# Optimization experiments

Measured on AMD Instinct MI355X. Metric: run time of the kernel, lower is better.

## Reference

```python
import jax, jax.numpy as jnp
import numpy as np

N_NODES = 50000
N_EDGES = 300000
D = 256          # in_dim = out_dim (residual)
DE = 256         # edge relation dim
K = 2            # num_kgs
H = 4            # heads
L = 2            # layers
DH = D // H


def _routed_linear(x, W, b, idx):
    # x:[E,din], W:[K,din,dout], b:[K,dout], idx:[E] in [0,K)
    # Compute all K branches (K is tiny) then select per edge.
    outs = jnp.einsum('ed,kdo->keo', x, W) + b[:, None, :]
    return outs[idx, jnp.arange(idx.shape[0])]


def _layernorm(x, g, b):
    mu = jnp.mean(x, axis=-1, keepdims=True)
    var = jnp.mean(jnp.square(x - mu), axis=-1, keepdims=True)
    return (x - mu) * jax.lax.rsqrt(var + 1e-5) * g + b


def _mga_layer(h, src, dst, kg_src, kg_dst, beta, rel,
               ln_g, ln_b, Wt, bt, Wq, bq, Wk, bk):
    N = h.shape[0]
    E = src.shape[0]
    residual = h
    hn = _layernorm(h, ln_g, ln_b)
    x_j = hn[src]                       # [E,D] gathered source feats
    x_i = hn[dst]                       # [E,D] gathered target feats
    # per-edge KG-routed transfer of concatenated (x_j, relation emb)
    xj_t = jax.nn.gelu(_routed_linear(jnp.concatenate([x_j, rel], axis=1), Wt, bt, kg_src),
                       approximate=False)
    q = _routed_linear(x_i, Wq, bq, kg_dst).reshape(E, H, DH)
    k = _routed_linear(xj_t, Wk, bk, kg_src).reshape(E, H, DH)
    # per-edge multi-head dot product, scaled by edge_beta_r then 1/sqrt(dh)
    att = jnp.sum(q * k, axis=-1) * beta[:, None] / jnp.sqrt(jnp.asarray(DH, h.dtype))  # [E,H]
    # scatter-softmax over incoming edges of each target node
    m = jax.ops.segment_max(att, dst, num_segments=N)          # [N,H]
    e = jnp.exp(att - m[dst])
    denom = jax.ops.segment_sum(e, dst, num_segments=N)        # [N,H]
    a = e / (denom[dst] + 1e-16)                                # [E,H]
    msg = (a[:, :, None] * xj_t.reshape(E, H, DH)).reshape(E, D)
    aggr = jax.ops.segment_sum(msg, dst, num_segments=N)        # [N,D]
    return residual + jax.nn.gelu(aggr, approximate=False)


def setup_inputs() -> dict:
    key = jax.random.key(0)
    ks = jax.random.split(key, 10)
    x = jax.random.normal(ks[0], (N_NODES, D), dtype=jnp.float32)
    edge_index = jax.random.randint(ks[1], (2, N_EDGES), 0, N_NODES, dtype=jnp.int32)
    edge_kg_index = jax.random.randint(ks[2], (2, N_EDGES), 0, K, dtype=jnp.int32)
    edge_beta_r = jax.random.uniform(ks[3], (N_EDGES,), dtype=jnp.float32)
    edge_rel_emb = jax.random.normal(ks[4], (N_EDGES, DE), dtype=jnp.float32)
    return {
        'x': x,
        'edge_index': edge_index,
        'edge_kg_index': edge_kg_index,
        'edge_beta_r': edge_beta_r,
        'edge_rel_emb': edge_rel_emb,
        'ln_g': jnp.ones((L, D), jnp.float32),
        'ln_b': jnp.zeros((L, D), jnp.float32),
        'Wt': jax.random.normal(ks[5], (L, K, D + DE, D), jnp.float32) / np.sqrt(D + DE),
        'bt': jnp.zeros((L, K, D), jnp.float32),
        'Wq': jax.random.normal(ks[6], (L, K, D, D), jnp.float32) / np.sqrt(D),
        'bq': jnp.zeros((L, K, D), jnp.float32),
        'Wk': jax.random.normal(ks[7], (L, K, D, D), jnp.float32) / np.sqrt(D),
        'bk': jnp.zeros((L, K, D), jnp.float32),
    }


def reference(x, edge_index, edge_kg_index, edge_beta_r, edge_rel_emb,
              ln_g, ln_b, Wt, bt, Wq, bq, Wk, bk):
    src, dst = edge_index[0], edge_index[1]          # j (source), i (target)
    kg_src, kg_dst = edge_kg_index[0], edge_kg_index[1]
    h = x  # dropout is identity in eval mode
    for l in range(L):
        h = _mga_layer(h, src, dst, kg_src, kg_dst, edge_beta_r, edge_rel_emb,
                       ln_g[l], ln_b[l], Wt[l], bt[l], Wq[l], bq[l], Wk[l], bk[l])
    return h
```

## Files before the change

### kernel.cpp

```cpp
#include <hip/hip_runtime.h>
#include <hip/hip_bf16.h>

#define NN 50000
#define NE 300000
#define DD 256
#define NCHUNK 293

typedef __hip_bfloat16 bf16;
typedef __attribute__((ext_vector_type(8))) short bf16x8;
typedef __attribute__((ext_vector_type(4))) float f32x4;

__device__ __forceinline__ float bf2f(bf16 v) { return __bfloat162float(v); }
__device__ __forceinline__ unsigned short f2b(float v) {
    bf16 t = __float2bfloat16(v);
    return *reinterpret_cast<unsigned short*>(&t);
}
__device__ __forceinline__ float b2f_bits(unsigned short u) {
    return __uint_as_float(((unsigned)u) << 16);
}
__device__ __forceinline__ float gelu_f(float v) {
    float v2 = v * v;
    float z  = v * fmaf(v2, 0.044715f, 1.0f) * 0.7978845608f;
    float e  = __expf(2.0f * z);
    float th = 1.0f - 2.0f / (e + 1.0f);
    return 0.5f * v * (1.0f + th);
}
__device__ __forceinline__ void gl2lds16(const uint4* g, uint4* l) {
    __builtin_amdgcn_global_load_lds(
        (const __attribute__((address_space(1))) void*)g,
        (__attribute__((address_space(3))) void*)l, 16, 0, 0);
}

__global__ void part_count(const int* __restrict__ kg, int* __restrict__ bcnt) {
    int base = blockIdx.x * 1024;
    __shared__ int wc[4];
    int t = threadIdx.x, wave = t >> 6, lane = t & 63;
    int cnt = 0;
    #pragma unroll
    for (int s = 0; s < 4; ++s) {
        int j = base + s * 256 + t;
        int is0 = (j < NE && kg[j] == 0) ? 1 : 0;
        unsigned long long m = __ballot(is0);
        if (lane == 0) cnt += __popcll(m);
    }
    if (lane == 0) wc[wave] = cnt;
    __syncthreads();
    if (t == 0) bcnt[blockIdx.x] = wc[0] + wc[1] + wc[2] + wc[3];
}

__global__ __launch_bounds__(512) void part_scan(const int* __restrict__ bcnt,
                                                 int* __restrict__ bofs,
                                                 int* __restrict__ meta, int n) {
    __shared__ int tmp[512];
    int t = threadIdx.x;
    int v = (t < n) ? bcnt[t] : 0;
    tmp[t] = v;
    __syncthreads();
    #pragma unroll
    for (int off = 1; off < 512; off <<= 1) {
        int u = (t >= off) ? tmp[t - off] : 0;
        __syncthreads();
        tmp[t] += u;
        __syncthreads();
    }
    if (t < n) bofs[t] = tmp[t] - v;
    if (t == n - 1) meta[0] = tmp[t];
}

__global__ void part_scatter(const int* __restrict__ kg, const int* __restrict__ bofs,
                             const int* __restrict__ meta, int* __restrict__ perm) {
    int base = blockIdx.x * 1024;
    int c0 = meta[0];
    __shared__ int wz[4];
    int t = threadIdx.x, wave = t >> 6, lane = t & 63;
    int zrun = bofs[blockIdx.x];
    for (int s = 0; s < 4; ++s) {
        int j = base + s * 256 + t;
        int valid = j < NE;
        int is0 = (valid && kg[j] == 0) ? 1 : 0;
        unsigned long long m = __ballot(is0);
        int zb = __popcll(m & ((1ull << lane) - 1ull));
        if (lane == 0) wz[wave] = __popcll(m);
        __syncthreads();
        int wbefore = 0;
        for (int w = 0; w < wave; ++w) wbefore += wz[w];
        int zeros_before = zrun + wbefore + zb;
        if (valid) {
            int pos = is0 ? zeros_before : (c0 + (j - zeros_before));
            perm[pos] = j;
        }
        int stepz = wz[0] + wz[1] + wz[2] + wz[3];
        __syncthreads();
        zrun += stepz;
    }
}

__global__ void deg_hist(const int* __restrict__ dst, int* __restrict__ deg) {
    int i = blockIdx.x * blockDim.x + threadIdx.x;
    if (i < NE) atomicAdd(&deg[dst[i]], 1);
}

__global__ __launch_bounds__(1024) void scan_big(const int* __restrict__ in,
                                                 int* __restrict__ ofs,
                                                 int* __restrict__ cur, int n) {
    __shared__ int part[1024];
    int t = threadIdx.x;
    int C = (n + 1023) >> 10;
    int base = t * C;
    int s = 0;
    for (int j = 0; j < C; ++j) { int idx = base + j; if (idx < n) s += in[idx]; }
    part[t] = s;
    __syncthreads();
    #pragma unroll
    for (int off = 1; off < 1024; off <<= 1) {
        int u = (t >= off) ? part[t - off] : 0;
        __syncthreads();
        part[t] += u;
        __syncthreads();
    }
    int run = (t == 0) ? 0 : part[t - 1];
    for (int j = 0; j < C; ++j) {
        int idx = base + j;
        if (idx < n) {
            ofs[idx] = run;
            if (cur) cur[idx] = run;
            run += in[idx];
        }
    }
    if (t == 1023) ofs[n] = part[1023];
}

__global__ void csr_fill(const int* __restrict__ dst, int* __restrict__ cur,
                         int* __restrict__ eid) {
    int i = blockIdx.x * blockDim.x + threadIdx.x;
    if (i < NE) {
        int p = atomicAdd(&cur[dst[i]], 1);
        eid[p] = i;
    }
}

__global__ void f2b_vec_kernel(const float* __restrict__ in, ushort* __restrict__ out, long n4) {
    long i0 = (long)blockIdx.x * blockDim.x + threadIdx.x;
    long stride = (long)gridDim.x * blockDim.x;
    for (long i = i0; i < n4; i += stride) {
        float4 v = ((const float4*)in)[i];
        ushort4 o;
        o.x = f2b(v.x); o.y = f2b(v.y); o.z = f2b(v.z); o.w = f2b(v.w);
        ((ushort4*)out)[i] = o;
    }
}

__global__ void transpose_w_kernel(const float* __restrict__ in, ushort* __restrict__ out,
                                   int shift, long total) {
    long i0 = (long)blockIdx.x * blockDim.x + threadIdx.x;
    long stride = (long)gridDim.x * blockDim.x;
    long dmask = ((long)1 << shift) - 1;
    for (long i = i0; i < total; i += stride) {
        long d = i & dmask;
        long rest = i >> shift;
        long o = rest & 255;
        long s = rest >> 8;
        out[i] = f2b(in[((s << shift) + d) * 256 + o]);
    }
}

__global__ void fill_kernel(float* __restrict__ p, float v, int n) {
    for (int i = blockIdx.x * blockDim.x + threadIdx.x; i < n; i += gridDim.x * blockDim.x)
        p[i] = v;
}

__global__ __launch_bounds__(256) void lnx_kernel(const float* __restrict__ x,
        const float* __restrict__ g, const float* __restrict__ b,
        float* __restrict__ h, bf16* __restrict__ hn) {
    int n = blockIdx.x * 4 + (threadIdx.x >> 6);
    if (n >= NN) return;
    int t = threadIdx.x & 63;
    float4 v = ((const float4*)(x + (size_t)n * DD))[t];
    ((float4*)(h + (size_t)n * DD))[t] = v;
    float s  = v.x + v.y + v.z + v.w;
    float s2 = v.x * v.x + v.y * v.y + v.z * v.z + v.w * v.w;
    #pragma unroll
    for (int off = 32; off; off >>= 1) {
        s  += __shfl_down(s, off);
        s2 += __shfl_down(s2, off);
    }
    s = __shfl(s, 0); s2 = __shfl(s2, 0);
    float mu  = s * (1.f / DD);
    float var = s2 * (1.f / DD) - mu * mu;
    float rs  = rsqrtf(var + 1e-5f);
    float vv[4] = {v.x, v.y, v.z, v.w};
    ushort4 pk;
    unsigned short* pku = (unsigned short*)&pk;
    #pragma unroll
    for (int j = 0; j < 4; ++j) {
        int c = t * 4 + j;
        pku[j] = f2b((vv[j] - mu) * rs * g[c] + b[c]);
    }
    ((ushort4*)(hn + (size_t)n * DD))[t] = pk;
}

__global__ __launch_bounds__(512) void nodeq_mfma(
        const bf16* __restrict__ hn,
        const ushort* __restrict__ WqT, const float* __restrict__ bq,
        const ushort* __restrict__ WtT, const float* __restrict__ bt,
        ushort* __restrict__ qn, ushort* __restrict__ hw) {
    __shared__ uint4 xh[64 * 32];
    __shared__ float bqs[2][256], bts[2][256];
    int t = threadIdx.x;
    int n0 = blockIdx.x * 64;
    int wave = t >> 6, lane = t & 63;
    if (t < 256) { bqs[0][t] = bq[t]; bqs[1][t] = bq[256 + t]; }
    else { int c = t & 255; bts[0][c] = bt[c]; bts[1][c] = bt[256 + c]; }
    const uint4* hn4 = (const uint4*)hn;
    #pragma unroll
    for (int j = 0; j < 4; ++j) {
        int pr = wave * 4 + j;
        int r2 = pr * 2 + (lane >> 5);
        int node = n0 + r2; if (node >= NN) node = NN - 1;
        int s = lane & 31;
        gl2lds16(hn4 + (size_t)node * 32 + (s ^ (r2 & 7)), &xh[pr * 64]);
    }
    __syncthreads();
    int lr = lane & 15, lg = lane >> 4;
    const char* xhb = (const char*)xh;
    f32x4 acc[2][2][4];
    #pragma unroll
    for (int b = 0; b < 2; ++b)
        #pragma unroll
        for (int m = 0; m < 2; ++m)
            #pragma unroll
            for (int n = 0; n < 4; ++n) acc[b][m][n] = (f32x4){0.f, 0.f, 0.f, 0.f};
    {
        const ushort* tr0 = WtT + (size_t)(wave * 32 + lr) * 512 + lg * 8;
        const ushort* tr1 = WtT + (size_t)(wave * 32 + 16 + lr) * 512 + lg * 8;
        #pragma unroll
        for (int kk = 0; kk < 8; ++kk) {
            bf16x8 a00 = *(const bf16x8*)(tr0 + kk * 32);
            bf16x8 a01 = *(const bf16x8*)(tr1 + kk * 32);
            bf16x8 a10 = *(const bf16x8*)(tr0 + 131072 + kk * 32);
            bf16x8 a11 = *(const bf16x8*)(tr1 + 131072 + kk * 32);
            bf16x8 bfr[4];
            #pragma unroll
            for (int n = 0; n < 4; ++n) {
                int r = n * 16 + lr;
                bfr[n] = *(const bf16x8*)(xhb + r * 512 + (((kk * 4 + lg) ^ (r & 7)) << 4));
            }
            #pragma unroll
            for (int n = 0; n < 4; ++n) {
                acc[0][0][n] = __builtin_amdgcn_mfma_f32_16x16x32_bf16(a00, bfr[n], acc[0][0][n], 0, 0, 0);
                acc[0][1][n] = __builtin_amdgcn_mfma_f32_16x16x32_bf16(a01, bfr[n], acc[0][1][n], 0, 0, 0);
                acc[1][0][n] = __builtin_amdgcn_mfma_f32_16x16x32_bf16(a10, bfr[n], acc[1][0][n], 0, 0, 0);
                acc[1][1][n] = __builtin_amdgcn_mfma_f32_16x16x32_bf16(a11, bfr[n], acc[1][1][n], 0, 0, 0);
            }
        }
    }
    #pragma unroll
    for (int n = 0; n < 4; ++n) {
        int e = n * 16 + lr;
        int node = n0 + e;
        if (node < NN) {
            #pragma unroll
            for (int br = 0; br < 2; ++br)
                #pragma unroll
                for (int m = 0; m < 2; ++m) {
                    int ob = wave * 32 + m * 16 + lg * 4;
                    f32x4 a = acc[br][m][n];
                    ushort4 pk;
                    unsigned short* pu = (unsigned short*)&pk;
                    #pragma unroll
                    for (int r = 0; r < 4; ++r) pu[r] = f2b(a[r] + bts[br][ob + r]);
                    *(ushort4*)(hw + ((size_t)br * NN + node) * 256 + ob) = pk;
                }
        }
    }
    #pragma unroll
    for (int b = 0; b < 2; ++b)
        #pragma unroll
        for (int m = 0; m < 2; ++m)
            #pragma unroll
            for (int n = 0; n < 4; ++n) acc[b][m][n] = (f32x4){0.f, 0.f, 0.f, 0.f};
    {
        const ushort* qr0 = WqT + (size_t)(wave * 32 + lr) * 256 + lg * 8;
        const ushort* qr1 = WqT + (size_t)(wave * 32 + 16 + lr) * 256 + lg * 8;
        #pragma unroll
        for (int kk = 0; kk < 8; ++kk) {
            bf16x8 a00 = *(const bf16x8*)(qr0 + kk * 32);
            bf16x8 a01 = *(const bf16x8*)(qr1 + kk * 32);
            bf16x8 a10 = *(const bf16x8*)(qr0 + 65536 + kk * 32);
            bf16x8 a11 = *(const bf16x8*)(qr1 + 65536 + kk * 32);
            bf16x8 bfr[4];
            #pragma unroll
            for (int n = 0; n < 4; ++n) {
                int r = n * 16 + lr;
                bfr[n] = *(const bf16x8*)(xhb + r * 512 + (((kk * 4 + lg) ^ (r & 7)) << 4));
            }
            #pragma unroll
            for (int n = 0; n < 4; ++n) {
                acc[0][0][n] = __builtin_amdgcn_mfma_f32_16x16x32_bf16(a00, bfr[n], acc[0][0][n], 0, 0, 0);
                acc[0][1][n] = __builtin_amdgcn_mfma_f32_16x16x32_bf16(a01, bfr[n], acc[0][1][n], 0, 0, 0);
                acc[1][0][n] = __builtin_amdgcn_mfma_f32_16x16x32_bf16(a10, bfr[n], acc[1][0][n], 0, 0, 0);
                acc[1][1][n] = __builtin_amdgcn_mfma_f32_16x16x32_bf16(a11, bfr[n], acc[1][1][n], 0, 0, 0);
            }
        }
    }
    #pragma unroll
    for (int n = 0; n < 4; ++n) {
        int e = n * 16 + lr;
        int node = n0 + e;
        if (node < NN) {
            #pragma unroll
            for (int br = 0; br < 2; ++br)
                #pragma unroll
                for (int m = 0; m < 2; ++m) {
                    int ob = wave * 32 + m * 16 + lg * 4;
                    f32x4 a = acc[br][m][n];
                    ushort4 pk;
                    unsigned short* pu = (unsigned short*)&pk;
                    #pragma unroll
                    for (int r = 0; r < 4; ++r) pu[r] = f2b(a[r] + bqs[br][ob + r]);
                    *(ushort4*)(qn + ((size_t)br * NN + node) * 256 + ob) = pk;
                }
        }
    }
}

template<int RELB>
__global__ __launch_bounds__(512, 4) void transfer_mfma(
        const float* __restrict__ rel, const ushort* __restrict__ relb,
        const int* __restrict__ src, const int* __restrict__ dst,
        const int* __restrict__ kgd,
        const int* __restrict__ perm, const int* __restrict__ meta,
        const ushort* __restrict__ WtT,
        const ushort* __restrict__ WkT, const float* __restrict__ bk,
        const ushort* __restrict__ qn, const ushort* __restrict__ hw,
        const float* __restrict__ beta,
        bf16* __restrict__ xjt, float* __restrict__ att) {
    __shared__ uint4 xr[64 * 32];
    __shared__ float bks[256];
    __shared__ float patt[8][64];
    __shared__ int sge[64], ssrc[64], sdst[64], sgd[64], sval[64];
    int t = threadIdx.x;
    int c0 = meta[0];
    int tiles0 = (c0 + 63) >> 6;
    int tiles1 = (NE - c0 + 63) >> 6;
    int bid = blockIdx.x;
    if (bid >= tiles0 + tiles1) return;
    int kgt, start, end;
    if (bid < tiles0) { kgt = 0; start = bid * 64; end = c0; }
    else              { kgt = 1; start = c0 + (bid - tiles0) * 64; end = NE; }
    int wave = t >> 6, lane = t & 63;
    if (t < 64) {
        int pos = start + t;
        int v = pos < end;
        int ge = perm[v ? pos : end - 1];
        sge[t] = ge; sval[t] = v; ssrc[t] = src[ge]; sdst[t] = dst[ge]; sgd[t] = kgd[ge];
    } else if (t >= 256) {
        bks[t - 256] = bk[kgt * 256 + (t - 256)];
    }
    __syncthreads();
    if (RELB) {
        const uint4* rb4 = (const uint4*)relb;
        #pragma unroll
        for (int j = 0; j < 4; ++j) {
            int pr = wave * 4 + j;
            int r2 = pr * 2 + (lane >> 5);
            int s = lane & 31;
            gl2lds16(rb4 + (size_t)sge[r2] * 32 + (s ^ (r2 & 7)), &xr[pr * 64]);
        }
    } else {
        #pragma unroll
        for (int i = 0; i < 8; ++i) {
            int r = i * 8 + wave;
            float4 f = ((const float4*)(rel + (size_t)sge[r] * 256))[lane];
            ushort4 o;
            o.x = f2b(f.x); o.y = f2b(f.y); o.z = f2b(f.z); o.w = f2b(f.w);
            int s = lane >> 1;
            char* bp = (char*)&xr[r * 32] + (((s ^ (r & 7)) << 4) | ((lane & 1) << 3));
            *(ushort4*)bp = o;
        }
    }
    int lr = lane & 15, lg = lane >> 4;
    f32x4 acc[2][4];
    #pragma unroll
    for (int n = 0; n < 4; ++n) {
        int e = n * 16 + lr;
        size_t hb = ((size_t)kgt * NN + ssrc[e]) * 256;
        #pragma unroll
        for (int m = 0; m < 2; ++m) {
            int ob = wave * 32 + m * 16 + lg * 4;
            ushort4 w4 = *(const ushort4*)(hw + hb + ob);
            acc[m][n] = (f32x4){b2f_bits(w4.x), b2f_bits(w4.y), b2f_bits(w4.z), b2f_bits(w4.w)};
        }
    }
    ushort4 kv[2][4];
    #pragma unroll
    for (int n = 0; n < 4; ++n) {
        int e = n * 16 + lr;
        size_t qb = ((size_t)sgd[e] * NN + sdst[e]) * 256;
        #pragma unroll
        for (int m = 0; m < 2; ++m) {
            int ob = wave * 32 + m * 16 + lg * 4;
            kv[m][n] = *(const ushort4*)(qn + qb + ob);
        }
    }
    __syncthreads();
    const char* xrb = (const char*)xr;
    const ushort* wb = WtT + (size_t)kgt * 131072;
    const ushort* wrow0 = wb + (size_t)(wave * 32 + lr) * 512 + 256 + lg * 8;
    const ushort* wrow1 = wb + (size_t)(wave * 32 + 16 + lr) * 512 + 256 + lg * 8;
    __builtin_amdgcn_s_setprio(1);
    #pragma unroll
    for (int kk = 0; kk < 8; ++kk) {
        bf16x8 a0 = *(const bf16x8*)(wrow0 + kk * 32);
        bf16x8 a1 = *(const bf16x8*)(wrow1 + kk * 32);
        bf16x8 bfr[4];
        #pragma unroll
        for (int n = 0; n < 4; ++n) {
            int r = n * 16 + lr;
            bfr[n] = *(const bf16x8*)(xrb + r * 512 + (((kk * 4 + lg) ^ (r & 7)) << 4));
        }
        #pragma unroll
        for (int m = 0; m < 2; ++m)
            #pragma unroll
            for (int n = 0; n < 4; ++n)
                acc[m][n] = __builtin_amdgcn_mfma_f32_16x16x32_bf16((m ? a1 : a0), bfr[n], acc[m][n], 0, 0, 0);
    }
    __builtin_amdgcn_s_setprio(0);
    __syncthreads();
    char* xob = (char*)xr;
    #pragma unroll
    for (int n = 0; n < 4; ++n) {
        int e = n * 16 + lr;
        #pragma unroll
        for (int m = 0; m < 2; ++m) {
            int ob = wave * 32 + m * 16 + lg * 4;
            f32x4 a = acc[m][n];
            ushort4 pk;
            unsigned short* pu = (unsigned short*)&pk;
            #pragma unroll
            for (int r = 0; r < 4; ++r)
                pu[r] = f2b(gelu_f(a[r]));
            int bofs = ob * 2;
            int slot = ((bofs >> 4) ^ (e & 7));
            *(ushort4*)(xob + e * 512 + slot * 16 + (bofs & 15)) = pk;
        }
    }
    __syncthreads();
    uint4* xjv = (uint4*)xjt;
    #pragma unroll
    for (int i = 0; i < 4; ++i) {
        int flat = i * 512 + t;
        int r = flat >> 5, c = flat & 31;
        if (sval[r])
            xjv[(size_t)sge[r] * 32 + c] = *(const uint4*)(xob + r * 512 + ((c ^ (r & 7)) << 4));
    }
    #pragma unroll
    for (int m = 0; m < 2; ++m)
        #pragma unroll
        for (int n = 0; n < 4; ++n) acc[m][n] = (f32x4){0.f, 0.f, 0.f, 0.f};
    const ushort* kbw = WkT + (size_t)kgt * 65536;
    const ushort* kr0 = kbw + (size_t)(wave * 32 + lr) * 256 + lg * 8;
    const ushort* kr1 = kbw + (size_t)(wave * 32 + 16 + lr) * 256 + lg * 8;
    __builtin_amdgcn_s_setprio(1);
    #pragma unroll
    for (int kk = 0; kk < 8; ++kk) {
        bf16x8 a0 = *(const bf16x8*)(kr0 + kk * 32);
        bf16x8 a1 = *(const bf16x8*)(kr1 + kk * 32);
        bf16x8 bfr[4];
        #pragma unroll
        for (int n = 0; n < 4; ++n) {
            int r = n * 16 + lr;
            bfr[n] = *(const bf16x8*)(xob + r * 512 + (((kk * 4 + lg) ^ (r & 7)) << 4));
        }
        #pragma unroll
        for (int n = 0; n < 4; ++n) {
            acc[0][n] = __builtin_amdgcn_mfma_f32_16x16x32_bf16(a0, bfr[n], acc[0][n], 0, 0, 0);
            acc[1][n] = __builtin_amdgcn_mfma_f32_16x16x32_bf16(a1, bfr[n], acc[1][n], 0, 0, 0);
        }
    }
    __builtin_amdgcn_s_setprio(0);
    float p[4];
    #pragma unroll
    for (int n = 0; n < 4; ++n) {
        float s = 0.f;
        #pragma unroll
        for (int m = 0; m < 2; ++m) {
            int ob = wave * 32 + m * 16 + lg * 4;
            ushort4 qv = kv[m][n];
            f32x4 kcv = acc[m][n];
            s = fmaf(b2f_bits(qv.x), kcv[0] + bks[ob + 0], s);
            s = fmaf(b2f_bits(qv.y), kcv[1] + bks[ob + 1], s);
            s = fmaf(b2f_bits(qv.z), kcv[2] + bks[ob + 2], s);
            s = fmaf(b2f_bits(qv.w), kcv[3] + bks[ob + 3], s);
        }
        p[n] = s;
    }
    #pragma unroll
    for (int n = 0; n < 4; ++n) {
        p[n] += __shfl_xor(p[n], 16);
        p[n] += __shfl_xor(p[n], 32);
    }
    if (lane < 16) {
        #pragma unroll
        for (int n = 0; n < 4; ++n) patt[wave][n * 16 + lr] = p[n];
    }
    __syncthreads();
    if (t < 256) {
        int e = t & 63, h = t >> 6;
        if (sval[e]) {
            int ge = sge[e];
            att[(size_t)ge * 4 + h] = (patt[2 * h][e] + patt[2 * h + 1][e]) * beta[ge] * 0.125f;
        }
    }
}

template<int WRITE_HN>
__global__ __launch_bounds__(256) void aggregate_kernel(
        const float* __restrict__ att, const bf16* __restrict__ xjt,
        const int* __restrict__ eid, const int* __restrict__ ofs,
        float* __restrict__ h, const float* __restrict__ g, const float* __restrict__ b,
        bf16* __restrict__ hn) {
    int node = blockIdx.x * 4 + (threadIdx.x >> 6);
    if (node >= NN) return;
    int lane = threadIdx.x & 63;
    int hh = lane >> 4;
    int beg = ofs[node], end = ofs[node + 1];
    float m = -1e30f, den = 0.f;
    float a0 = 0.f, a1 = 0.f, a2 = 0.f, a3 = 0.f;
    for (int i = beg; i < end; ++i) {
        int e = eid[i];
        float av = att[(size_t)e * 4 + hh];
        if (av > m) {
            float r = __expf(m - av);
            den *= r; a0 *= r; a1 *= r; a2 *= r; a3 *= r;
            m = av;
        }
        float wgt = __expf(av - m);
        den += wgt;
        ushort4 v = *(const ushort4*)((const ushort*)xjt + (size_t)e * 256 + lane * 4);
        a0 = fmaf(wgt, b2f_bits(v.x), a0);
        a1 = fmaf(wgt, b2f_bits(v.y), a1);
        a2 = fmaf(wgt, b2f_bits(v.z), a2);
        a3 = fmaf(wgt, b2f_bits(v.w), a3);
    }
    float inv = 1.f / (den + 1e-16f);
    float4 hv = ((float4*)(h + (size_t)node * 256))[lane];
    hv.x += gelu_f(a0 * inv);
    hv.y += gelu_f(a1 * inv);
    hv.z += gelu_f(a2 * inv);
    hv.w += gelu_f(a3 * inv);
    ((float4*)(h + (size_t)node * 256))[lane] = hv;
    if (WRITE_HN) {
        float s  = hv.x + hv.y + hv.z + hv.w;
        float s2 = hv.x * hv.x + hv.y * hv.y + hv.z * hv.z + hv.w * hv.w;
        #pragma unroll
        for (int off = 32; off; off >>= 1) {
            s  += __shfl_down(s, off);
            s2 += __shfl_down(s2, off);
        }
        s = __shfl(s, 0); s2 = __shfl(s2, 0);
        float mu  = s * (1.f / DD);
        float var = s2 * (1.f / DD) - mu * mu;
        float rs  = rsqrtf(var + 1e-5f);
        float vv[4] = {hv.x, hv.y, hv.z, hv.w};
        ushort4 pk;
        unsigned short* pku = (unsigned short*)&pk;
        #pragma unroll
        for (int j = 0; j < 4; ++j) {
            int c = lane * 4 + j;
            pku[j] = f2b((vv[j] - mu) * rs * g[c] + b[c]);
        }
        ((ushort4*)(hn + (size_t)node * DD))[lane] = pk;
    }
}

extern "C" void kernel_launch(void* const* d_in, const int* in_sizes, int n_in,
                              void* d_out, int out_size, void* d_ws, size_t ws_size,
                              hipStream_t stream) {
    const float* x    = (const float*)d_in[0];
    const int*   ei   = (const int*)d_in[1];
    const int*   ekg  = (const int*)d_in[2];
    const float* beta = (const float*)d_in[3];
    const float* rel  = (const float*)d_in[4];
    const float* ln_g = (const float*)d_in[5];
    const float* ln_b = (const float*)d_in[6];
    const float* Wt   = (const float*)d_in[7];
    const float* bt   = (const float*)d_in[8];
    const float* Wq   = (const float*)d_in[9];
    const float* bq   = (const float*)d_in[10];
    const float* Wk   = (const float*)d_in[11];
    const float* bk   = (const float*)d_in[12];

    float* h = (float*)d_out;

    const int* srcp = ei;
    const int* dstp = ei + NE;
    const int* kgs  = ekg;
    const int* kgd  = ekg + NE;

    char* w = (char*)d_ws;
    float*  att   = (float*)w;  w += (size_t)NE * 4 * 4;
    bf16*   hn    = (bf16*)w;   w += (size_t)NN * DD * 2;
    bf16*   xjt   = (bf16*)w;   w += (size_t)NE * DD * 2;
    ushort* qn    = (ushort*)w; w += (size_t)2 * NN * DD * 2;
    ushort* hw    = (ushort*)w; w += (size_t)2 * NN * DD * 2;
    ushort* WtT   = (ushort*)w; w += (size_t)4 * 256 * 512 * 2;
    ushort* WqT   = (ushort*)w; w += (size_t)4 * 256 * 256 * 2;
    ushort* WkT   = (ushort*)w; w += (size_t)4 * 256 * 256 * 2;
    int* perm_src = (int*)w;    w += (size_t)NE * 4;
    int* bcnt0    = (int*)w;    w += NCHUNK * 4;
    int* bofs0    = (int*)w;    w += NCHUNK * 4;
    int* meta0    = (int*)w;    w += 64;
    int* deg      = (int*)w;    w += (size_t)NN * 4;
    int* ofs      = (int*)w;    w += (size_t)(NN + 1) * 4;
    int* cur      = (int*)w;    w += (size_t)NN * 4;
    int* eid      = (int*)w;    w += (size_t)NE * 4;
    size_t used = (size_t)(w - (char*)d_ws);
    ushort* relb = (ushort*)w;
    int use_relb = (ws_size >= used + (size_t)NE * DD * 2) ? 1 : 0;

    part_count<<<NCHUNK, 256, 0, stream>>>(kgs, bcnt0);
    part_scan<<<1, 512, 0, stream>>>(bcnt0, bofs0, meta0, NCHUNK);
    part_scatter<<<NCHUNK, 256, 0, stream>>>(kgs, bofs0, meta0, perm_src);

    fill_kernel<<<64, 256, 0, stream>>>((float*)deg, 0.f, NN);
    deg_hist<<<(NE + 255) / 256, 256, 0, stream>>>(dstp, deg);
    scan_big<<<1, 1024, 0, stream>>>(deg, ofs, cur, NN);
    csr_fill<<<(NE + 255) / 256, 256, 0, stream>>>(dstp, cur, eid);

    if (use_relb)
        f2b_vec_kernel<<<2048, 256, 0, stream>>>(rel, relb, (long)NE * DD / 4);
    transpose_w_kernel<<<512, 256, 0, stream>>>(Wt, WtT, 9, (long)4 * 256 * 512);
    transpose_w_kernel<<<256, 256, 0, stream>>>(Wq, WqT, 8, (long)4 * 256 * 256);
    transpose_w_kernel<<<256, 256, 0, stream>>>(Wk, WkT, 8, (long)4 * 256 * 256);

    const int EBP = (NE + 126) / 64;
    const int QB  = (NN + 63) / 64;
    const int AGB = (NN + 3) / 4;

    lnx_kernel<<<AGB, 256, 0, stream>>>(x, ln_g, ln_b, h, hn);
    for (int l = 0; l < 2; ++l) {
        nodeq_mfma<<<QB, 512, 0, stream>>>(hn,
                WqT + (size_t)l * 2 * 256 * 256, bq + l * 512,
                WtT + (size_t)l * 2 * 256 * 512, bt + l * 512, qn, hw);
        if (use_relb)
            transfer_mfma<1><<<EBP, 512, 0, stream>>>(rel, relb, srcp, dstp, kgd,
                    perm_src, meta0,
                    WtT + (size_t)l * 2 * 256 * 512,
                    WkT + (size_t)l * 2 * 256 * 256, bk + l * 512, qn, hw, beta, xjt, att);
        else
            transfer_mfma<0><<<EBP, 512, 0, stream>>>(rel, relb, srcp, dstp, kgd,
                    perm_src, meta0,
                    WtT + (size_t)l * 2 * 256 * 512,
                    WkT + (size_t)l * 2 * 256 * 256, bk + l * 512, qn, hw, beta, xjt, att);
        if (l == 0)
            aggregate_kernel<1><<<AGB, 256, 0, stream>>>(att, xjt, eid, ofs, h,
                    ln_g + DD, ln_b + DD, hn);
        else
            aggregate_kernel<0><<<AGB, 256, 0, stream>>>(att, xjt, eid, ofs, h,
                    ln_g, ln_b, hn);
    }
}
```

Baseline: 1.165 ms.

## Pre-permute edge data and write transfer outputs in CSR order

Edge metadata, beta and bf16 relation embeddings are pre-permuted into the KG-sorted order, so the transfer kernel reads them contiguously instead of through the permutation. Transfer results (xjt, att) are written directly at each edge's CSR position, so the aggregate kernel streams them sequentially without the eid indirection. The transfer kernel's output writes become scattered, and several small setup kernels and workspace arrays are added.

```diff
diff --git a/kernel.cpp b/kernel.cpp
--- a/kernel.cpp
+++ b/kernel.cpp
@@ -130,24 +130,40 @@
     if (t == 1023) ofs[n] = part[1023];
 }
 
-__global__ void csr_fill(const int* __restrict__ dst, int* __restrict__ cur,
-                         int* __restrict__ eid) {
+__global__ void csr_fill_ipos(const int* __restrict__ dst, int* __restrict__ cur,
+                              int* __restrict__ ipos) {
     int i = blockIdx.x * blockDim.x + threadIdx.x;
     if (i < NE) {
         int p = atomicAdd(&cur[dst[i]], 1);
-        eid[p] = i;
-    }
-}
-
-__global__ void f2b_vec_kernel(const float* __restrict__ in, ushort* __restrict__ out, long n4) {
-    long i0 = (long)blockIdx.x * blockDim.x + threadIdx.x;
-    long stride = (long)gridDim.x * blockDim.x;
-    for (long i = i0; i < n4; i += stride) {
-        float4 v = ((const float4*)in)[i];
-        ushort4 o;
-        o.x = f2b(v.x); o.y = f2b(v.y); o.z = f2b(v.z); o.w = f2b(v.w);
-        ((ushort4*)out)[i] = o;
-    }
+        ipos[i] = p;
+    }
+}
+
+__global__ void build_perm_arrays(const int* __restrict__ perm,
+        const int* __restrict__ src, const int* __restrict__ dst,
+        const int* __restrict__ kgd, const int* __restrict__ ipos,
+        int* __restrict__ src_p, int* __restrict__ dst_p,
+        int* __restrict__ kgd_p, int* __restrict__ ipos_p) {
+    int i = blockIdx.x * blockDim.x + threadIdx.x;
+    if (i < NE) {
+        int ge = perm[i];
+        src_p[i] = src[ge];
+        dst_p[i] = dst[ge];
+        kgd_p[i] = kgd[ge];
+        ipos_p[i] = ipos[ge];
+    }
+}
+
+__global__ __launch_bounds__(256) void f2b_perm_kernel(const float* __restrict__ rel,
+        const int* __restrict__ perm, ushort* __restrict__ relb) {
+    int row = blockIdx.x * 4 + (threadIdx.x >> 6);
+    if (row >= NE) return;
+    int lane = threadIdx.x & 63;
+    int ge = perm[row];
+    float4 f = ((const float4*)(rel + (size_t)ge * 256))[lane];
+    ushort4 o;
+    o.x = f2b(f.x); o.y = f2b(f.y); o.z = f2b(f.z); o.w = f2b(f.w);
+    ((ushort4*)(relb + (size_t)row * 256))[lane] = o;
 }
 
 __global__ void transpose_w_kernel(const float* __restrict__ in, ushort* __restrict__ out,
@@ -327,18 +343,19 @@
 template<int RELB>
 __global__ __launch_bounds__(512, 4) void transfer_mfma(
         const float* __restrict__ rel, const ushort* __restrict__ relb,
-        const int* __restrict__ src, const int* __restrict__ dst,
-        const int* __restrict__ kgd,
-        const int* __restrict__ perm, const int* __restrict__ meta,
+        const int* __restrict__ perm,
+        const int* __restrict__ src_p, const int* __restrict__ dst_p,
+        const int* __restrict__ kgd_p, const int* __restrict__ ipos_p,
+        const int* __restrict__ meta,
         const ushort* __restrict__ WtT,
         const ushort* __restrict__ WkT, const float* __restrict__ bk,
         const ushort* __restrict__ qn, const ushort* __restrict__ hw,
-        const float* __restrict__ beta,
+        const float* __restrict__ beta_p, const float* __restrict__ beta,
         bf16* __restrict__ xjt, float* __restrict__ att) {
     __shared__ uint4 xr[64 * 32];
     __shared__ float bks[256];
     __shared__ float patt[8][64];
-    __shared__ int sge[64], ssrc[64], sdst[64], sgd[64], sval[64];
+    __shared__ int ssrc[64], sdst[64], sgd[64], sip[64], sval[64];
     int t = threadIdx.x;
     int c0 = meta[0];
     int tiles0 = (c0 + 63) >> 6;
@@ -352,8 +369,12 @@
     if (t < 64) {
         int pos = start + t;
         int v = pos < end;
-        int ge = perm[v ? pos : end - 1];
-        sge[t] = ge; sval[t] = v; ssrc[t] = src[ge]; sdst[t] = dst[ge]; sgd[t] = kgd[ge];
+        int cp = v ? pos : end - 1;
+        sval[t] = v;
+        ssrc[t] = src_p[cp];
+        sdst[t] = dst_p[cp];
+        sgd[t]  = kgd_p[cp];
+        sip[t]  = ipos_p[cp];
     } else if (t >= 256) {
         bks[t - 256] = bk[kgt * 256 + (t - 256)];
     }
@@ -364,14 +385,17 @@
         for (int j = 0; j < 4; ++j) {
             int pr = wave * 4 + j;
             int r2 = pr * 2 + (lane >> 5);
+            int rp = start + r2; if (rp >= end) rp = end - 1;
             int s = lane & 31;
-            gl2lds16(rb4 + (size_t)sge[r2] * 32 + (s ^ (r2 & 7)), &xr[pr * 64]);
+            gl2lds16(rb4 + (size_t)rp * 32 + (s ^ (r2 & 7)), &xr[pr * 64]);
         }
     } else {
         #pragma unroll
         for (int i = 0; i < 8; ++i) {
             int r = i * 8 + wave;
-            float4 f = ((const float4*)(rel + (size_t)sge[r] * 256))[lane];
+            int rp = start + r; if (rp >= end) rp = end - 1;
+            int ge = perm[rp];
+            float4 f = ((const float4*)(rel + (size_t)ge * 256))[lane];
             ushort4 o;
             o.x = f2b(f.x); o.y = f2b(f.y); o.z = f2b(f.z); o.w = f2b(f.w);
             int s = lane >> 1;
@@ -452,7 +476,7 @@
         int flat = i * 512 + t;
         int r = flat >> 5, c = flat & 31;
         if (sval[r])
-            xjv[(size_t)sge[r] * 32 + c] = *(const uint4*)(xob + r * 512 + ((c ^ (r & 7)) << 4));
+            xjv[(size_t)sip[r] * 32 + c] = *(const uint4*)(xob + r * 512 + ((c ^ (r & 7)) << 4));
     }
     #pragma unroll
     for (int m = 0; m < 2; ++m)
@@ -508,8 +532,9 @@
     if (t < 256) {
         int e = t & 63, h = t >> 6;
         if (sval[e]) {
-            int ge = sge[e];
-            att[(size_t)ge * 4 + h] = (patt[2 * h][e] + patt[2 * h + 1][e]) * beta[ge] * 0.125f;
+            int pos = start + e;
+            float bv = beta_p[pos];
+            att[(size_t)sip[e] * 4 + h] = (patt[2 * h][e] + patt[2 * h + 1][e]) * bv * 0.125f;
         }
     }
 }
@@ -517,7 +542,7 @@
 template<int WRITE_HN>
 __global__ __launch_bounds__(256) void aggregate_kernel(
         const float* __restrict__ att, const bf16* __restrict__ xjt,
-        const int* __restrict__ eid, const int* __restrict__ ofs,
+        const int* __restrict__ ofs,
         float* __restrict__ h, const float* __restrict__ g, const float* __restrict__ b,
         bf16* __restrict__ hn) {
     int node = blockIdx.x * 4 + (threadIdx.x >> 6);
@@ -528,8 +553,7 @@
     float m = -1e30f, den = 0.f;
     float a0 = 0.f, a1 = 0.f, a2 = 0.f, a3 = 0.f;
     for (int i = beg; i < end; ++i) {
-        int e = eid[i];
-        float av = att[(size_t)e * 4 + hh];
+        float av = att[(size_t)i * 4 + hh];
         if (av > m) {
             float r = __expf(m - av);
             den *= r; a0 *= r; a1 *= r; a2 *= r; a3 *= r;
@@ -537,7 +561,7 @@
         }
         float wgt = __expf(av - m);
         den += wgt;
-        ushort4 v = *(const ushort4*)((const ushort*)xjt + (size_t)e * 256 + lane * 4);
+        ushort4 v = *(const ushort4*)((const ushort*)xjt + (size_t)i * 256 + lane * 4);
         a0 = fmaf(wgt, b2f_bits(v.x), a0);
         a1 = fmaf(wgt, b2f_bits(v.y), a1);
         a2 = fmaf(wgt, b2f_bits(v.z), a2);
@@ -572,6 +596,12 @@
         }
         ((ushort4*)(hn + (size_t)node * DD))[lane] = pk;
     }
+}
+
+__global__ void beta_perm_kernel(const float* __restrict__ beta, const int* __restrict__ perm,
+                                 float* __restrict__ beta_p) {
+    int i = blockIdx.x * blockDim.x + threadIdx.x;
+    if (i < NE) beta_p[i] = beta[perm[i]];
 }
 
 extern "C" void kernel_launch(void* const* d_in, const int* in_sizes, int n_in,
@@ -614,7 +644,12 @@
     int* deg      = (int*)w;    w += (size_t)NN * 4;
     int* ofs      = (int*)w;    w += (size_t)(NN + 1) * 4;
     int* cur      = (int*)w;    w += (size_t)NN * 4;
-    int* eid      = (int*)w;    w += (size_t)NE * 4;
+    int* ipos     = (int*)w;    w += (size_t)NE * 4;
+    int* src_p    = (int*)w;    w += (size_t)NE * 4;
+    int* dst_p    = (int*)w;    w += (size_t)NE * 4;
+    int* kgd_p    = (int*)w;    w += (size_t)NE * 4;
+    int* ipos_p   = (int*)w;    w += (size_t)NE * 4;
+    float* beta_p = (float*)w;  w += (size_t)NE * 4;
     size_t used = (size_t)(w - (char*)d_ws);
     ushort* relb = (ushort*)w;
     int use_relb = (ws_size >= used + (size_t)NE * DD * 2) ? 1 : 0;
@@ -626,10 +661,14 @@
     fill_kernel<<<64, 256, 0, stream>>>((float*)deg, 0.f, NN);
     deg_hist<<<(NE + 255) / 256, 256, 0, stream>>>(dstp, deg);
     scan_big<<<1, 1024, 0, stream>>>(deg, ofs, cur, NN);
-    csr_fill<<<(NE + 255) / 256, 256, 0, stream>>>(dstp, cur, eid);
+    csr_fill_ipos<<<(NE + 255) / 256, 256, 0, stream>>>(dstp, cur, ipos);
+
+    build_perm_arrays<<<(NE + 255) / 256, 256, 0, stream>>>(perm_src, srcp, dstp, kgd, ipos,
+            src_p, dst_p, kgd_p, ipos_p);
+    beta_perm_kernel<<<(NE + 255) / 256, 256, 0, stream>>>(beta, perm_src, beta_p);
 
     if (use_relb)
-        f2b_vec_kernel<<<2048, 256, 0, stream>>>(rel, relb, (long)NE * DD / 4);
+        f2b_perm_kernel<<<(NE + 3) / 4, 256, 0, stream>>>(rel, perm_src, relb);
     transpose_w_kernel<<<512, 256, 0, stream>>>(Wt, WtT, 9, (long)4 * 256 * 512);
     transpose_w_kernel<<<256, 256, 0, stream>>>(Wq, WqT, 8, (long)4 * 256 * 256);
     transpose_w_kernel<<<256, 256, 0, stream>>>(Wk, WkT, 8, (long)4 * 256 * 256);
@@ -644,20 +683,20 @@
                 WqT + (size_t)l * 2 * 256 * 256, bq + l * 512,
                 WtT + (size_t)l * 2 * 256 * 512, bt + l * 512, qn, hw);
         if (use_relb)
-            transfer_mfma<1><<<EBP, 512, 0, stream>>>(rel, relb, srcp, dstp, kgd,
-                    perm_src, meta0,
+            transfer_mfma<1><<<EBP, 512, 0, stream>>>(rel, relb, perm_src,
+                    src_p, dst_p, kgd_p, ipos_p, meta0,
                     WtT + (size_t)l * 2 * 256 * 512,
-                    WkT + (size_t)l * 2 * 256 * 256, bk + l * 512, qn, hw, beta, xjt, att);
+                    WkT + (size_t)l * 2 * 256 * 256, bk + l * 512, qn, hw, beta_p, beta, xjt, att);
         else
-            transfer_mfma<0><<<EBP, 512, 0, stream>>>(rel, relb, srcp, dstp, kgd,
-                    perm_src, meta0,
+            transfer_mfma<0><<<EBP, 512, 0, stream>>>(rel, relb, perm_src,
+                    src_p, dst_p, kgd_p, ipos_p, meta0,
                     WtT + (size_t)l * 2 * 256 * 512,
-                    WkT + (size_t)l * 2 * 256 * 256, bk + l * 512, qn, hw, beta, xjt, att);
+                    WkT + (size_t)l * 2 * 256 * 256, bk + l * 512, qn, hw, beta_p, beta, xjt, att);
         if (l == 0)
-            aggregate_kernel<1><<<AGB, 256, 0, stream>>>(att, xjt, eid, ofs, h,
+            aggregate_kernel<1><<<AGB, 256, 0, stream>>>(att, xjt, ofs, h,
                     ln_g + DD, ln_b + DD, hn);
         else
-            aggregate_kernel<0><<<AGB, 256, 0, stream>>>(att, xjt, eid, ofs, h,
+            aggregate_kernel<0><<<AGB, 256, 0, stream>>>(att, xjt, ofs, h,
                     ln_g, ln_b, hn);
     }
 }
```

New measurement: 1.123 ms. 1.04x faster.
